# Kernel optimization log

Measured on AMD Instinct MI355X. Metric: run time of the kernel, lower is better.

The kernel has to match this reference:

```python
import jax, jax.numpy as jnp
import numpy as np
from jax import lax

ENC_DIM, DEC_DIM, ATT_DIM, CONV_CH, KSIZE, ATT_ODIM = 1024, 1024, 512, 32, 50, 1024
SCALING = 2.0


def setup_inputs() -> dict:
    key = jax.random.key(0)
    ks = jax.random.split(key, 12)
    B, T = 32, 2000
    enc_pad = jax.random.normal(ks[0], (B, T, ENC_DIM), dtype=jnp.float32)
    enc_len = jax.random.randint(ks[1], (B,), 1000, T + 1, dtype=jnp.int32)
    dec_h = jax.random.normal(ks[2], (B, 1, DEC_DIM), dtype=jnp.float32)
    att_prev = jax.random.uniform(ks[3], (B, T), dtype=jnp.float32)
    s = 0.02
    W_enc = jax.random.normal(ks[4], (ENC_DIM, ATT_DIM), dtype=jnp.float32) * s
    b_enc = jnp.zeros((ATT_DIM,), jnp.float32)
    W_dec = jax.random.normal(ks[5], (DEC_DIM, ATT_DIM), dtype=jnp.float32) * s
    b_dec = jnp.zeros((ATT_DIM,), jnp.float32)
    W_att = jax.random.normal(ks[6], (CONV_CH, ATT_DIM), dtype=jnp.float32) * s
    b_att = jnp.zeros((ATT_DIM,), jnp.float32)
    # Conv2d(1, C, kernel=(1, 2K+1)) acting on (B,1,1,T) == 1D conv kernel (C,1,2K+1)
    conv_w = jax.random.normal(ks[7], (CONV_CH, 1, 2 * KSIZE + 1), dtype=jnp.float32) * s
    gvec = jax.random.normal(ks[8], (ATT_DIM, 1), dtype=jnp.float32) * s
    W_o = jax.random.normal(ks[9], (ENC_DIM, ATT_ODIM), dtype=jnp.float32) * s
    b_o = jnp.zeros((ATT_ODIM,), jnp.float32)
    return {"enc_pad": enc_pad, "enc_len": enc_len, "dec_h": dec_h, "att_prev": att_prev,
            "W_enc": W_enc, "b_enc": b_enc, "W_dec": W_dec, "b_dec": b_dec,
            "W_att": W_att, "b_att": b_att, "conv_w": conv_w, "gvec": gvec,
            "W_o": W_o, "b_o": b_o}


def reference(enc_pad, enc_len, dec_h, att_prev, W_enc, b_enc, W_dec, b_dec,
              W_att, b_att, conv_w, gvec, W_o, b_o):
    B, T, _ = enc_pad.shape
    enc_h = enc_pad @ W_enc + b_enc                           # [B,T,A]
    # location conv: (B,1,T) * (C,1,K) -> (B,C,T), SAME padding
    att_conv = lax.conv_general_dilated(
        att_prev[:, None, :], conv_w, window_strides=(1,),
        padding=[(KSIZE, KSIZE)], dimension_numbers=("NCH", "OIH", "NCH"))
    att_conv = jnp.transpose(att_conv, (0, 2, 1)) @ W_att + b_att  # [B,T,A]
    dec_term = (dec_h.reshape(B, DEC_DIM) @ W_dec + b_dec)[:, None, :]  # [B,1,A]
    att_state = jnp.tanh(enc_h + dec_term + att_conv)         # [B,T,A]
    e = (att_state @ gvec)[:, :, 0]                           # [B,T]
    mask = jnp.arange(T)[None, :] >= enc_len[:, None]         # True = padded
    e = jnp.where(mask, jnp.float32(-1e15), e)
    attn = jax.nn.softmax(SCALING * e, axis=1)                # [B,T]
    c = jnp.einsum("bt,btd->bd", attn, enc_pad)               # [B,enc_dim]
    c = c @ W_o + b_o                                         # [B,att_odim]
    return c, attn
```

## Files before the change

### kernel.cpp

```cpp
#include <hip/hip_runtime.h>
#include <stdint.h>
#include <stddef.h>

#define T_LEN   2000
#define BATCH   32
#define ROWS    64000
#define KDIM    1024
#define ADIM    512
#define CCH     32
#define KW      101

typedef _Float16 half8_t  __attribute__((ext_vector_type(8)));
typedef float    float4_t __attribute__((ext_vector_type(4)));

__device__ __forceinline__ half8_t pack8(float4_t a, float4_t b) {
    half8_t r;
    r[0] = (_Float16)a.x; r[1] = (_Float16)a.y;
    r[2] = (_Float16)a.z; r[3] = (_Float16)a.w;
    r[4] = (_Float16)b.x; r[5] = (_Float16)b.y;
    r[6] = (_Float16)b.z; r[7] = (_Float16)b.w;
    return r;
}

__device__ __forceinline__ float tanh_fast(float x) {
    float ax = __builtin_fabsf(x);
    ax = fminf(ax, 15.f);
    float e = __expf(2.f * ax);
    float t = 1.f - 2.f * __builtin_amdgcn_rcpf(e + 1.f);
    return (x < 0.f) ? -t : t;
}

__device__ __forceinline__ void glds16(const void* g, void* l) {
    __builtin_amdgcn_global_load_lds((const __attribute__((address_space(1))) uint32_t*)g,
                                     (__attribute__((address_space(3))) uint32_t*)l,
                                     16, 0, 0);
}

#define OFF_WENCT 0
#define OFF_WATTT 1048576
#define OFF_CONVA 1081344
#define OFF_DTERM 9273344
#define OFF_EPART 9338880
#define OFF_CPART 10362880

__global__ __launch_bounds__(256) void k_prep(const float* __restrict__ We,
                                              const float* __restrict__ Wa,
                                              const float* __restrict__ dec_h,
                                              const float* __restrict__ W_dec,
                                              const float* __restrict__ be,
                                              const float* __restrict__ bd,
                                              const float* __restrict__ ba,
                                              const float* __restrict__ att_prev,
                                              const float* __restrict__ conv_w,
                                              _Float16* __restrict__ Wet,
                                              _Float16* __restrict__ Wat,
                                              float* __restrict__ dterm,
                                              float* __restrict__ convA) {
    __shared__ float smem[3460];
    const int blk = blockIdx.x, tid = threadIdx.x;

    if (blk < 512) {
        float (*tile)[33] = (float(*)[33])smem;
        const int k0 = (blk >> 4) * 32, n0 = (blk & 15) * 32;
        const int tx = tid & 31, ty = tid >> 5;
#pragma unroll
        for (int i = 0; i < 4; ++i)
            tile[ty + i * 8][tx] = We[(size_t)(k0 + ty + i * 8) * ADIM + n0 + tx];
        __syncthreads();
#pragma unroll
        for (int i = 0; i < 4; ++i)
            Wet[(size_t)(n0 + ty + i * 8) * KDIM + k0 + tx] = (_Float16)tile[tx][ty + i * 8];
    } else if (blk < 640) {
        float* dh = smem;
        float* part = smem + 1024;
        const int idx = blk - 512, b = idx >> 2, a0 = (idx & 3) * 128;
#pragma unroll
        for (int i = 0; i < 4; ++i) dh[tid + i * 256] = dec_h[b * KDIM + tid + i * 256];
        __syncthreads();
        const int a = a0 + (tid & 127), kh = (tid >> 7) * 512;
        float s = 0.f;
#pragma unroll 8
        for (int k = 0; k < 512; ++k) s += dh[kh + k] * W_dec[(size_t)(kh + k) * ADIM + a];
        part[tid] = s;
        __syncthreads();
        if (tid < 128) {
            const int aa = a0 + tid;
            dterm[b * ADIM + aa] = part[tid] + part[tid + 128] + be[aa] + bd[aa] + ba[aa];
        }
    } else if (blk < 1152) {
        float* ap = smem;
        float* w  = smem + 228;
        const int idx = blk - 640, b = idx >> 4, tt = idx & 15;
        const int t0 = tt * 128;
        for (int i = tid; i < 228; i += 256) {
            int t = t0 - 50 + i;
            ap[i] = (t >= 0 && t < T_LEN) ? att_prev[b * T_LEN + t] : 0.f;
        }
        for (int i = tid; i < CCH * KW; i += 256) w[i] = conv_w[i];
        __syncthreads();
        for (int idx2 = tid; idx2 < 128 * CCH; idx2 += 256) {
            int tl = idx2 >> 5, c = idx2 & 31;
            int t = t0 + tl;
            if (t < T_LEN) {
                float s = 0.f;
#pragma unroll
                for (int j = 0; j < KW; ++j) s += ap[tl + j] * w[c * KW + j];
                convA[(size_t)(b * T_LEN + t) * CCH + c] = s;
            }
        }
    } else {
#pragma unroll
        for (int rr = 0; rr < 2; ++rr) {
            const int n = tid * 2 + rr;
#pragma unroll
            for (int c = 0; c < CCH; ++c)
                Wat[n * CCH + c] = (_Float16)Wa[c * ADIM + n];
        }
    }
}

__global__ __launch_bounds__(256, 3) void k_gemm_e(const float* __restrict__ enc,
                                                   const _Float16* __restrict__ Wet,
                                                   const float* __restrict__ convA,
                                                   const _Float16* __restrict__ Wat,
                                                   const float* __restrict__ dterm,
                                                   const float* __restrict__ gvec,
                                                   float* __restrict__ epart) {
    __shared__ __attribute__((aligned(16))) float    Af[2][128 * 32];
    __shared__ __attribute__((aligned(16))) _Float16 Bh[2][128 * 32];

    const int tid  = threadIdx.x;
    const int nc   = blockIdx.x, m0 = blockIdx.y * 128, n0 = nc * 128;
    const int wave = tid >> 6, lane = tid & 63;
    const int quad = lane >> 4, c16 = lane & 15;
    const int wm = (wave >> 1) * 64, wn = (wave & 1) * 64;

    const int rlA = lane >> 3, segA = lane & 7;
    const int rlB = lane >> 2, segB = lane & 3;
    const int aOff = ((segA - rlA) & 7) * 4;
    const int bOff = ((segB - ((rlB >> 1) & 3)) & 3) * 8;

    const float*    aG = enc + (size_t)(m0 + wave * 32 + rlA) * KDIM + aOff;
    const _Float16* bG = Wet + (size_t)(n0 + wave * 32 + rlB) * KDIM + bOff;
    const float*    aC = convA + (size_t)(m0 + wave * 32 + rlA) * CCH + aOff;
    const _Float16* bC = Wat + (size_t)(n0 + wave * 32 + rlB) * CCH + bOff;

    const int aR0 = ((c16 + quad * 2 + 0) & 7) * 4;
    const int aR1 = ((c16 + quad * 2 + 1) & 7) * 4;
    const int bR  = ((quad + (c16 >> 1)) & 3) * 8;

    float g[4], dt0[4], dt1[4];
    const int b0 = m0 / T_LEN, b1 = (m0 + 127) / T_LEN;
    const int lim = (b0 + 1) * T_LEN;
#pragma unroll
    for (int j = 0; j < 4; ++j) {
        const int col = n0 + wn + j * 16 + c16;
        g[j]   = gvec[col];
        dt0[j] = dterm[b0 * ADIM + col];
        dt1[j] = dterm[b1 * ADIM + col];
    }

    float4_t acc[4][4];
#pragma unroll
    for (int i = 0; i < 4; ++i)
#pragma unroll
        for (int j = 0; j < 4; ++j) acc[i][j] = (float4_t){0.f, 0.f, 0.f, 0.f};

#pragma unroll
    for (int i = 0; i < 4; ++i)
        glds16(aG + (size_t)i * 8 * KDIM, &Af[0][(wave * 32 + i * 8) * 32]);
#pragma unroll
    for (int i = 0; i < 2; ++i)
        glds16(bG + (size_t)i * 16 * KDIM, &Bh[0][(wave * 32 + i * 16) * 32]);
    __syncthreads();

    for (int kk = 0; kk < 33; ++kk) {
        const int cur = kk & 1, nxt = cur ^ 1;
        if (kk < 32) {
            if (kk + 1 < 32) {
                const int kn = (kk + 1) * 32;
#pragma unroll
                for (int i = 0; i < 4; ++i)
                    glds16(aG + (size_t)i * 8 * KDIM + kn, &Af[nxt][(wave * 32 + i * 8) * 32]);
#pragma unroll
                for (int i = 0; i < 2; ++i)
                    glds16(bG + (size_t)i * 16 * KDIM + kn, &Bh[nxt][(wave * 32 + i * 16) * 32]);
            } else {
#pragma unroll
                for (int i = 0; i < 4; ++i)
                    glds16(aC + (size_t)i * 8 * CCH, &Af[nxt][(wave * 32 + i * 8) * 32]);
#pragma unroll
                for (int i = 0; i < 2; ++i)
                    glds16(bC + (size_t)i * 16 * CCH, &Bh[nxt][(wave * 32 + i * 16) * 32]);
            }
        }
        half8_t af[4], bf[4];
#pragma unroll
        for (int i = 0; i < 4; ++i) {
            const float* base = &Af[cur][(wm + i * 16 + c16) * 32];
            float4_t u0 = *(const float4_t*)(base + aR0);
            float4_t u1 = *(const float4_t*)(base + aR1);
            af[i] = pack8(u0, u1);
        }
#pragma unroll
        for (int j = 0; j < 4; ++j)
            bf[j] = *(const half8_t*)&Bh[cur][(wn + j * 16 + c16) * 32 + bR];
#pragma unroll
        for (int i = 0; i < 4; ++i)
#pragma unroll
            for (int j = 0; j < 4; ++j)
                acc[i][j] = __builtin_amdgcn_mfma_f32_16x16x32_f16(af[i], bf[j], acc[i][j], 0, 0, 0);
        __syncthreads();
    }

    float* e_lds = (float*)&Bh[0][0];
#pragma unroll
    for (int i = 0; i < 4; ++i) {
#pragma unroll
        for (int r = 0; r < 4; ++r) {
            const int rloc = wm + i * 16 + quad * 4 + r;
            const bool hi = (m0 + rloc) >= lim;
            float s = 0.f;
#pragma unroll
            for (int j = 0; j < 4; ++j)
                s += tanh_fast(acc[i][j][r] + (hi ? dt1[j] : dt0[j])) * g[j];
#pragma unroll
            for (int off = 1; off < 16; off <<= 1) s += __shfl_xor(s, off);
            if (c16 == 0) e_lds[rloc * 2 + (wave & 1)] = s;
        }
    }
    __syncthreads();
    if (tid < 128) {
        const float2 q = ((const float2*)e_lds)[tid];
        epart[nc * ROWS + m0 + tid] = q.x + q.y;
    }
}

__global__ __launch_bounds__(512) void k_softmax(const float* __restrict__ epart,
                                                 const int* __restrict__ enc_len,
                                                 float* __restrict__ attn) {
    __shared__ float ex[T_LEN];
    __shared__ float red[8];
    const int b = blockIdx.x, tid = threadIdx.x;
    const int len = enc_len[b];
    float lmax = -3.4e38f;
    for (int t = tid; t < T_LEN; t += 512) {
        float e = epart[b * T_LEN + t] + epart[ROWS + b * T_LEN + t]
                + epart[2 * ROWS + b * T_LEN + t] + epart[3 * ROWS + b * T_LEN + t];
        float lg = (t < len) ? 2.f * e : -2e15f;
        ex[t] = lg;
        lmax = fmaxf(lmax, lg);
    }
    for (int off = 1; off < 64; off <<= 1) lmax = fmaxf(lmax, __shfl_xor(lmax, off));
    if ((tid & 63) == 0) red[tid >> 6] = lmax;
    __syncthreads();
    const float m = fmaxf(fmaxf(fmaxf(red[0], red[1]), fmaxf(red[2], red[3])),
                          fmaxf(fmaxf(red[4], red[5]), fmaxf(red[6], red[7])));
    float lsum = 0.f;
    for (int t = tid; t < T_LEN; t += 512) {
        float p = __expf(ex[t] - m);
        ex[t] = p;
        lsum += p;
    }
    for (int off = 1; off < 64; off <<= 1) lsum += __shfl_xor(lsum, off);
    __syncthreads();
    if ((tid & 63) == 0) red[tid >> 6] = lsum;
    __syncthreads();
    const float inv = 1.f / (red[0] + red[1] + red[2] + red[3] + red[4] + red[5] + red[6] + red[7]);
    for (int t = tid; t < T_LEN; t += 512) attn[b * T_LEN + t] = ex[t] * inv;
}

__global__ __launch_bounds__(256) void k_cpart(const float* __restrict__ attn,
                                               const float* __restrict__ enc,
                                               float* __restrict__ cpart) {
    const int b = blockIdx.y, tc = blockIdx.x, tid = threadIdx.x;
    const int t0 = tc * 125;
    float4_t s = (float4_t){0.f, 0.f, 0.f, 0.f};
    const float4_t* ep = (const float4_t*)(enc + (size_t)b * T_LEN * KDIM) + tid;
    const float* ap = attn + b * T_LEN + t0;
#pragma unroll 5
    for (int tt = 0; tt < 125; ++tt) {
        const float w = ap[tt];
        float4_t v = ep[(size_t)(t0 + tt) * 256];
        s += v * w;
    }
    *(float4_t*)&cpart[(size_t)(tc * BATCH + b) * KDIM + tid * 4] = s;
}

__global__ __launch_bounds__(256) void k_out(const float* __restrict__ cpart,
                                             const float* __restrict__ W_o,
                                             const float* __restrict__ b_o,
                                             float* __restrict__ out_c) {
    __shared__ float cm[KDIM];
    const int b = blockIdx.x, tid = threadIdx.x;
    for (int d = tid; d < KDIM; d += 256) {
        float s = 0.f;
#pragma unroll
        for (int p = 0; p < 16; ++p) s += cpart[(size_t)(p * BATCH + b) * KDIM + d];
        cm[d] = s;
    }
    __syncthreads();
    const int o = blockIdx.y * 256 + tid;
    float s = b_o[o];
#pragma unroll 8
    for (int d = 0; d < KDIM; ++d) s += cm[d] * W_o[(size_t)d * KDIM + o];
    out_c[b * KDIM + o] = s;
}

extern "C" void kernel_launch(void* const* d_in, const int* in_sizes, int n_in,
                              void* d_out, int out_size, void* d_ws, size_t ws_size,
                              hipStream_t stream) {
    const float* enc      = (const float*)d_in[0];
    const int*   enc_len  = (const int*)d_in[1];
    const float* dec_h    = (const float*)d_in[2];
    const float* att_prev = (const float*)d_in[3];
    const float* W_enc    = (const float*)d_in[4];
    const float* b_enc    = (const float*)d_in[5];
    const float* W_dec    = (const float*)d_in[6];
    const float* b_dec    = (const float*)d_in[7];
    const float* W_att    = (const float*)d_in[8];
    const float* b_att    = (const float*)d_in[9];
    const float* conv_w   = (const float*)d_in[10];
    const float* gvec     = (const float*)d_in[11];
    const float* W_o      = (const float*)d_in[12];
    const float* b_o      = (const float*)d_in[13];

    float* out_c    = (float*)d_out;
    float* out_attn = out_c + BATCH * KDIM;

    char* ws = (char*)d_ws;
    _Float16* Wet    = (_Float16*)(ws + OFF_WENCT);
    _Float16* Wat    = (_Float16*)(ws + OFF_WATTT);
    float*    convAF = (float*)(ws + OFF_CONVA);
    float*    dterm  = (float*)(ws + OFF_DTERM);
    float*    epart  = (float*)(ws + OFF_EPART);
    float*    cpart  = (float*)(ws + OFF_CPART);

    k_prep<<<1153, 256, 0, stream>>>(W_enc, W_att, dec_h, W_dec, b_enc, b_dec, b_att,
                                     att_prev, conv_w, Wet, Wat, dterm, convAF);
    k_gemm_e<<<dim3(4, 500), 256, 0, stream>>>(enc, Wet, convAF, Wat, dterm, gvec, epart);
    k_softmax<<<BATCH, 512, 0, stream>>>(epart, enc_len, out_attn);
    k_cpart<<<dim3(16, BATCH), 256, 0, stream>>>(out_attn, enc, cpart);
    k_out<<<dim3(BATCH, 4), 256, 0, stream>>>(cpart, W_o, b_o, out_c);
}
```

Baseline: 657.6 us.

## Pre-convert encoder to fp16 in workspace and run GEMM/context on half data

Adds a prep pass that converts the full fp32 encoder tensor to fp16 in workspace when the workspace is large enough. The GEMM then stages half A tiles, which halves LDS use and allows higher occupancy, and the context reduction reads fp16 too. Block order is also remapped to group M tiles across the N chunks, and LDS staging layouts change. The extra conversion pass reads 256MB and writes 128MB, which may cost more than the savings, and the context vector loses precision because it is computed from fp16 encoder values.

New measurement: 611.1 us. 1.08x faster.

```diff
diff --git a/kernel.cpp b/kernel.cpp
--- a/kernel.cpp
+++ b/kernel.cpp
@@ -11,6 +11,7 @@
 #define KW      101
 
 typedef _Float16 half8_t  __attribute__((ext_vector_type(8)));
+typedef _Float16 half4_t  __attribute__((ext_vector_type(4)));
 typedef float    float4_t __attribute__((ext_vector_type(4)));
 
 __device__ __forceinline__ half8_t pack8(float4_t a, float4_t b) {
@@ -38,10 +39,14 @@
 
 #define OFF_WENCT 0
 #define OFF_WATTT 1048576
-#define OFF_CONVA 1081344
-#define OFF_DTERM 9273344
-#define OFF_EPART 9338880
-#define OFF_CPART 10362880
+#define OFF_CONV  1081344
+#define M_DTERM   5177344
+#define M_EPART   5242880
+#define M_CPART   6266880
+#define M_ENCH    8364032
+#define F_DTERM   9273344
+#define F_EPART   9338880
+#define F_CPART   10362880
 
 __global__ __launch_bounds__(256) void k_prep(const float* __restrict__ We,
                                               const float* __restrict__ Wa,
@@ -52,13 +57,23 @@
                                               const float* __restrict__ ba,
                                               const float* __restrict__ att_prev,
                                               const float* __restrict__ conv_w,
+                                              const float* __restrict__ enc,
                                               _Float16* __restrict__ Wet,
                                               _Float16* __restrict__ Wat,
                                               float* __restrict__ dterm,
-                                              float* __restrict__ convA) {
+                                              void* __restrict__ convO,
+                                              _Float16* __restrict__ encH,
+                                              int f16mode) {
     __shared__ float smem[3460];
     const int blk = blockIdx.x, tid = threadIdx.x;
 
+    if (blk >= 1153) {
+        const size_t idx = (size_t)(blk - 1153) * 2048 + tid * 8;
+        const float4_t* s = (const float4_t*)(enc + idx);
+        float4_t v0 = s[0], v1 = s[1];
+        *(half8_t*)(encH + idx) = pack8(v0, v1);
+        return;
+    }
     if (blk < 512) {
         float (*tile)[33] = (float(*)[33])smem;
         const int k0 = (blk >> 4) * 32, n0 = (blk & 15) * 32;
@@ -105,7 +120,9 @@
                 float s = 0.f;
 #pragma unroll
                 for (int j = 0; j < KW; ++j) s += ap[tl + j] * w[c * KW + j];
-                convA[(size_t)(b * T_LEN + t) * CCH + c] = s;
+                const size_t o = (size_t)(b * T_LEN + t) * CCH + c;
+                if (f16mode) ((_Float16*)convO)[o] = (_Float16)s;
+                else         ((float*)convO)[o] = s;
             }
         }
     } else {
@@ -119,35 +136,44 @@
     }
 }
 
-__global__ __launch_bounds__(256, 3) void k_gemm_e(const float* __restrict__ enc,
-                                                   const _Float16* __restrict__ Wet,
-                                                   const float* __restrict__ convA,
-                                                   const _Float16* __restrict__ Wat,
-                                                   const float* __restrict__ dterm,
-                                                   const float* __restrict__ gvec,
-                                                   float* __restrict__ epart) {
-    __shared__ __attribute__((aligned(16))) float    Af[2][128 * 32];
+template<bool F16A>
+__global__ __launch_bounds__(256, F16A ? 4 : 3)
+void k_gemm_e(const void* __restrict__ encv,
+              const _Float16* __restrict__ Wet,
+              const void* __restrict__ convv,
+              const _Float16* __restrict__ Wat,
+              const float* __restrict__ dterm,
+              const float* __restrict__ gvec,
+              float* __restrict__ epart) {
+    constexpr int ABYTES = F16A ? 8192 : 16384;
+    __shared__ __attribute__((aligned(16))) char     Ab[2][ABYTES];
     __shared__ __attribute__((aligned(16))) _Float16 Bh[2][128 * 32];
 
     const int tid  = threadIdx.x;
-    const int nc   = blockIdx.x, m0 = blockIdx.y * 128, n0 = nc * 128;
+    const int blk  = blockIdx.x;
+    int nc, mt;
+    if (blk < 1984) { nc = (blk >> 3) & 3; mt = (blk >> 5) * 8 + (blk & 7); }
+    else            { int r = blk - 1984; nc = r >> 2; mt = 496 + (r & 3); }
+    const int m0 = mt * 128, n0 = nc * 128;
+
     const int wave = tid >> 6, lane = tid & 63;
     const int quad = lane >> 4, c16 = lane & 15;
     const int wm = (wave >> 1) * 64, wn = (wave & 1) * 64;
 
-    const int rlA = lane >> 3, segA = lane & 7;
-    const int rlB = lane >> 2, segB = lane & 3;
-    const int aOff = ((segA - rlA) & 7) * 4;
-    const int bOff = ((segB - ((rlB >> 1) & 3)) & 3) * 8;
-
-    const float*    aG = enc + (size_t)(m0 + wave * 32 + rlA) * KDIM + aOff;
-    const _Float16* bG = Wet + (size_t)(n0 + wave * 32 + rlB) * KDIM + bOff;
-    const float*    aC = convA + (size_t)(m0 + wave * 32 + rlA) * CCH + aOff;
-    const _Float16* bC = Wat + (size_t)(n0 + wave * 32 + rlB) * CCH + bOff;
-
-    const int aR0 = ((c16 + quad * 2 + 0) & 7) * 4;
-    const int aR1 = ((c16 + quad * 2 + 1) & 7) * 4;
-    const int bR  = ((quad + (c16 >> 1)) & 3) * 8;
+    const int rlB = lane & 15, sgB = lane >> 4;
+    const int rlA = F16A ? (lane & 15) : (lane & 7);
+    const int sgA = F16A ? (lane >> 4) : (lane >> 3);
+    constexpr int AISS = F16A ? 2 : 4;
+    constexpr int ARPC = F16A ? 16 : 8;
+    constexpr int AEPS = F16A ? 8 : 4;
+
+    const _Float16* encH = (const _Float16*)encv;
+    const float*    encF = (const float*)encv;
+    const _Float16* cvH  = (const _Float16*)convv;
+    const float*    cvF  = (const float*)convv;
+
+    const size_t aRow = (size_t)(m0 + wave * 32 + rlA);
+    const size_t bRow = (size_t)(n0 + wave * 32 + rlB);
 
     float g[4], dt0[4], dt1[4];
     const int b0 = m0 / T_LEN, b1 = (m0 + 127) / T_LEN;
@@ -166,45 +192,55 @@
 #pragma unroll
         for (int j = 0; j < 4; ++j) acc[i][j] = (float4_t){0.f, 0.f, 0.f, 0.f};
 
-#pragma unroll
-    for (int i = 0; i < 4; ++i)
-        glds16(aG + (size_t)i * 8 * KDIM, &Af[0][(wave * 32 + i * 8) * 32]);
-#pragma unroll
-    for (int i = 0; i < 2; ++i)
-        glds16(bG + (size_t)i * 16 * KDIM, &Bh[0][(wave * 32 + i * 16) * 32]);
+#define STAGE_A(buf, base, stride, k0)                                              \
+    _Pragma("unroll")                                                               \
+    for (int i = 0; i < AISS; ++i)                                                  \
+        glds16((base) + ((aRow + i * ARPC) * (stride)) + (k0) + sgA * AEPS,         \
+               &Ab[buf][(wave * AISS + i) * 1024]);
+#define STAGE_B(buf, base, stride, k0)                                              \
+    _Pragma("unroll")                                                               \
+    for (int i = 0; i < 2; ++i)                                                     \
+        glds16((base) + ((bRow + i * 16) * (stride)) + (k0) + sgB * 8,              \
+               (char*)&Bh[buf][0] + (wave * 2 + i) * 1024);
+
+    if (F16A) { STAGE_A(0, encH, KDIM, 0) } else { STAGE_A(0, encF, KDIM, 0) }
+    STAGE_B(0, Wet, KDIM, 0)
     __syncthreads();
 
     for (int kk = 0; kk < 33; ++kk) {
         const int cur = kk & 1, nxt = cur ^ 1;
-        if (kk < 32) {
-            if (kk + 1 < 32) {
-                const int kn = (kk + 1) * 32;
-#pragma unroll
-                for (int i = 0; i < 4; ++i)
-                    glds16(aG + (size_t)i * 8 * KDIM + kn, &Af[nxt][(wave * 32 + i * 8) * 32]);
-#pragma unroll
-                for (int i = 0; i < 2; ++i)
-                    glds16(bG + (size_t)i * 16 * KDIM + kn, &Bh[nxt][(wave * 32 + i * 16) * 32]);
-            } else {
-#pragma unroll
-                for (int i = 0; i < 4; ++i)
-                    glds16(aC + (size_t)i * 8 * CCH, &Af[nxt][(wave * 32 + i * 8) * 32]);
-#pragma unroll
-                for (int i = 0; i < 2; ++i)
-                    glds16(bC + (size_t)i * 16 * CCH, &Bh[nxt][(wave * 32 + i * 16) * 32]);
+        if (kk < 31) {
+            const int kn = (kk + 1) * 32;
+            if (F16A) { STAGE_A(nxt, encH, KDIM, kn) } else { STAGE_A(nxt, encF, KDIM, kn) }
+            STAGE_B(nxt, Wet, KDIM, kn)
+        } else if (kk == 31) {
+            if (F16A) { STAGE_A(nxt, cvH, CCH, 0) } else { STAGE_A(nxt, cvF, CCH, 0) }
+            STAGE_B(nxt, Wat, CCH, 0)
+        }
+        half8_t af[4], bf[4];
+        if (F16A) {
+            const _Float16* Ah = (const _Float16*)Ab[cur];
+#pragma unroll
+            for (int i = 0; i < 4; ++i) {
+                const int row = wm + i * 16 + c16;
+                af[i] = *(const half8_t*)(Ah + (row >> 4) * 512 + (quad * 16 + c16) * 8);
             }
-        }
-        half8_t af[4], bf[4];
-#pragma unroll
-        for (int i = 0; i < 4; ++i) {
-            const float* base = &Af[cur][(wm + i * 16 + c16) * 32];
-            float4_t u0 = *(const float4_t*)(base + aR0);
-            float4_t u1 = *(const float4_t*)(base + aR1);
-            af[i] = pack8(u0, u1);
-        }
-#pragma unroll
-        for (int j = 0; j < 4; ++j)
-            bf[j] = *(const half8_t*)&Bh[cur][(wn + j * 16 + c16) * 32 + bR];
+        } else {
+            const float* Afp = (const float*)Ab[cur];
+#pragma unroll
+            for (int i = 0; i < 4; ++i) {
+                const int row = wm + i * 16 + c16;
+                const float* cb = Afp + (row >> 3) * 256 + (row & 7) * 4;
+                float4_t u0 = *(const float4_t*)(cb + (2 * quad) * 32);
+                float4_t u1 = *(const float4_t*)(cb + (2 * quad + 1) * 32);
+                af[i] = pack8(u0, u1);
+            }
+        }
+#pragma unroll
+        for (int j = 0; j < 4; ++j) {
+            const int row = wn + j * 16 + c16;
+            bf[j] = *(const half8_t*)(&Bh[cur][0] + (row >> 4) * 512 + (quad * 16 + c16) * 8);
+        }
 #pragma unroll
         for (int i = 0; i < 4; ++i)
 #pragma unroll
@@ -234,6 +270,8 @@
         const float2 q = ((const float2*)e_lds)[tid];
         epart[nc * ROWS + m0 + tid] = q.x + q.y;
     }
+#undef STAGE_A
+#undef STAGE_B
 }
 
 __global__ __launch_bounds__(512) void k_softmax(const float* __restrict__ epart,
@@ -270,9 +308,27 @@
     for (int t = tid; t < T_LEN; t += 512) attn[b * T_LEN + t] = ex[t] * inv;
 }
 
-__global__ __launch_bounds__(256) void k_cpart(const float* __restrict__ attn,
-                                               const float* __restrict__ enc,
-                                               float* __restrict__ cpart) {
+__global__ __launch_bounds__(256) void k_cpart_h(const float* __restrict__ attn,
+                                                 const _Float16* __restrict__ encH,
+                                                 float* __restrict__ cpart) {
+    const int b = blockIdx.y, tc = blockIdx.x, tid = threadIdx.x;
+    const int t0 = tc * 125;
+    float4_t s = (float4_t){0.f, 0.f, 0.f, 0.f};
+    const half4_t* ep = (const half4_t*)(encH + (size_t)b * T_LEN * KDIM) + tid;
+    const float* ap = attn + b * T_LEN + t0;
+#pragma unroll 5
+    for (int tt = 0; tt < 125; ++tt) {
+        const float w = ap[tt];
+        half4_t v = ep[(size_t)(t0 + tt) * 256];
+        s.x += w * (float)v[0]; s.y += w * (float)v[1];
+        s.z += w * (float)v[2]; s.w += w * (float)v[3];
+    }
+    *(float4_t*)&cpart[(size_t)(tc * BATCH + b) * KDIM + tid * 4] = s;
+}
+
+__global__ __launch_bounds__(256) void k_cpart_f(const float* __restrict__ attn,
+                                                 const float* __restrict__ enc,
+                                                 float* __restrict__ cpart) {
     const int b = blockIdx.y, tc = blockIdx.x, tid = threadIdx.x;
     const int t0 = tc * 125;
     float4_t s = (float4_t){0.f, 0.f, 0.f, 0.f};
@@ -329,17 +385,38 @@
     float* out_attn = out_c + BATCH * KDIM;
 
     char* ws = (char*)d_ws;
-    _Float16* Wet    = (_Float16*)(ws + OFF_WENCT);
-    _Float16* Wat    = (_Float16*)(ws + OFF_WATTT);
-    float*    convAF = (float*)(ws + OFF_CONVA);
-    float*    dterm  = (float*)(ws + OFF_DTERM);
-    float*    epart  = (float*)(ws + OFF_EPART);
-    float*    cpart  = (float*)(ws + OFF_CPART);
-
-    k_prep<<<1153, 256, 0, stream>>>(W_enc, W_att, dec_h, W_dec, b_enc, b_dec, b_att,
-                                     att_prev, conv_w, Wet, Wat, dterm, convAF);
-    k_gemm_e<<<dim3(4, 500), 256, 0, stream>>>(enc, Wet, convAF, Wat, dterm, gvec, epart);
-    k_softmax<<<BATCH, 512, 0, stream>>>(epart, enc_len, out_attn);
-    k_cpart<<<dim3(16, BATCH), 256, 0, stream>>>(out_attn, enc, cpart);
-    k_out<<<dim3(BATCH, 4), 256, 0, stream>>>(cpart, W_o, b_o, out_c);
-}
+    _Float16* Wet = (_Float16*)(ws + OFF_WENCT);
+    _Float16* Wat = (_Float16*)(ws + OFF_WATTT);
+
+    const size_t needMain = (size_t)M_ENCH + (size_t)ROWS * KDIM * 2;
+    const bool f16p = ws_size >= needMain;
+
+    if (f16p) {
+        _Float16* convH = (_Float16*)(ws + OFF_CONV);
+        float*    dterm = (float*)(ws + M_DTERM);
+        float*    epart = (float*)(ws + M_EPART);
+        float*    cpart = (float*)(ws + M_CPART);
+        _Float16* encH  = (_Float16*)(ws + M_ENCH);
+
+        k_prep<<<1153 + 32000, 256, 0, stream>>>(W_enc, W_att, dec_h, W_dec, b_enc, b_dec,
+                                                 b_att, att_prev, conv_w, enc,
+                                                 Wet, Wat, dterm, convH, encH, 1);
+        k_gemm_e<true><<<2000, 256, 0, stream>>>(encH, Wet, convH, Wat, dterm, gvec, epart);
+        k_softmax<<<BATCH, 512, 0, stream>>>(epart, enc_len, out_attn);
+        k_cpart_h<<<dim3(16, BATCH), 256, 0, stream>>>(out_attn, encH, cpart);
+        k_out<<<dim3(BATCH, 4), 256, 0, stream>>>(cpart, W_o, b_o, out_c);
+    } else {
+        float* convF = (float*)(ws + OFF_CONV);
+        float* dterm = (float*)(ws + F_DTERM);
+        float* epart = (float*)(ws + F_EPART);
+        float* cpart = (float*)(ws + F_CPART);
+
+        k_prep<<<1153, 256, 0, stream>>>(W_enc, W_att, dec_h, W_dec, b_enc, b_dec,
+                                         b_att, att_prev, conv_w, enc,
+                                         Wet, Wat, dterm, convF, (_Float16*)nullptr, 0);
+        k_gemm_e<false><<<2000, 256, 0, stream>>>(enc, Wet, convF, Wat, dterm, gvec, epart);
+        k_softmax<<<BATCH, 512, 0, stream>>>(epart, enc_len, out_attn);
+        k_cpart_f<<<dim3(16, BATCH), 256, 0, stream>>>(out_attn, enc, cpart);
+        k_out<<<dim3(BATCH, 4), 256, 0, stream>>>(cpart, W_o, b_o, out_c);
+    }
+}
```
